# Optimization experiments

Hardware: AMD Instinct MI355X
Metric: run time of the kernel (lower is better)

## Reference

```python
import jax, jax.numpy as jnp
import numpy as np

N, D = 32, 16  # output capsules, output capsule dim
J, I = 16, 8   # input capsules, input capsule dim
B = 16384

def setup_inputs() -> dict:
    key = jax.random.key(0)
    k1, k2 = jax.random.split(key)
    inputs = jax.random.normal(k1, (B, J, I), dtype=jnp.float32)
    # kaiming_normal_ on (N,16,8,D): fan_in computed from dims -> std = sqrt(2/fan_in)
    fan_in = I * D  # torch fan_in for a 4D tensor (N,16,8,D) is dim1*receptive? faithful scale: gain*sqrt(1/fan)
    W = jax.random.normal(k2, (N, J, I, D), dtype=jnp.float32) * np.float32(np.sqrt(2.0 / (J * I * D / N if False else fan_in)))
    b = jnp.zeros((N, J, 1), dtype=jnp.float32)
    return {"inputs": inputs, "W": W, "b": b}

def reference(inputs, W, b):
    # pose transform: u[b,n,j,z] = sum_i inputs[b,j,i] * W[n,j,i,z]
    u = jnp.einsum('bji,njiz->bnjz', inputs, W)          # (B, N, J, D)
    # self-agreement: c[b,n,i] = sum_{k,j} u[b,n,i,j] * u[b,n,k,j]
    c = jnp.einsum('bnij,bnj->bni', u, u.sum(axis=-2))   # (B, N, J)
    c = c[..., None] / jnp.sqrt(jnp.float32(D))          # (B, N, J, 1)
    c = jax.nn.softmax(c, axis=1)                        # softmax over N axis (torch dim=1)
    c = c + b                                            # broadcast (N, J, 1)
    s = jnp.sum(u * c, axis=-2)                          # (B, N, D)
    return s
```

## Files before the change

### kernel.cpp

```cpp
#include <hip/hip_runtime.h>

#define B_TOT 16384
#define TBB   16
#define NTH   512
#define SLS   524

typedef short bf16x8 __attribute__((ext_vector_type(8)));
typedef float f32x4  __attribute__((ext_vector_type(4)));
union U4 { bf16x8 v; uint4 q; };

__device__ __forceinline__ unsigned f2bf(float f) {
    unsigned u = __float_as_uint(f);
    return (u + 0x7fffu + ((u >> 16) & 1u)) >> 16;
}

__device__ __forceinline__ uint4 packrow(const float* src) {
    uint4 o;
    o.x = f2bf(src[0])  | (f2bf(src[16])  << 16);
    o.y = f2bf(src[32]) | (f2bf(src[48])  << 16);
    o.z = f2bf(src[64]) | (f2bf(src[80])  << 16);
    o.w = f2bf(src[96]) | (f2bf(src[112]) << 16);
    return o;
}

__global__ void prepack(const float* __restrict__ W, uint4* __restrict__ Wp)
{
    const int t = blockIdx.x * 256 + threadIdx.x;
    const int lane = t & 63, s = (t >> 6) & 3, n = t >> 8;
    const int q = lane >> 4, z = lane & 15;
    Wp[t] = packrow(W + (size_t)(n * 16 + 4 * s + q) * 128 + z);
}

__global__ __launch_bounds__(NTH, 8)
void caps(const float* __restrict__ X, const uint4* __restrict__ Wp,
          const float* __restrict__ Bias, float* __restrict__ Out)
{
    __shared__ __align__(16) float sL[TBB * SLS];
    __shared__ float sBias[512];

    const int t    = threadIdx.x;
    const int lane = t & 63;
    const int wv   = t >> 6;
    const int b16  = lane & 15;
    const int q    = lane >> 4;
    const long bb  = (long)blockIdx.x * TBB;

    sBias[t] = Bias[t];

    unsigned moct[4];
    #pragma unroll
    for (int c = 0; c < 4; ++c) moct[c] = (q == c) ? 0xffffffffu : 0u;

    uint4 xq[4];
    #pragma unroll
    for (int s = 0; s < 4; ++s) {
        const float* xs = X + (bb + b16) * 128 + (4 * s + q) * 8;
        float4 a = *reinterpret_cast<const float4*>(xs);
        float4 c = *reinterpret_cast<const float4*>(xs + 4);
        uint4 o;
        o.x = f2bf(a.x) | (f2bf(a.y) << 16);
        o.y = f2bf(a.z) | (f2bf(a.w) << 16);
        o.z = f2bf(c.x) | (f2bf(c.y) << 16);
        o.w = f2bf(c.z) | (f2bf(c.w) << 16);
        xq[s] = o;
    }

    const f32x4 zero4 = {0.f, 0.f, 0.f, 0.f};

    auto maskA = [&](const uint4& wkf, int c) {
        U4 a;
        const unsigned m = moct[c];
        a.q.x = wkf.x & m; a.q.y = wkf.y & m;
        a.q.z = wkf.z & m; a.q.w = wkf.w & m;
        return a;
    };

    uint4 wk[4];

    #pragma unroll 1
    for (int nq = 0; nq < 4; ++nq) {
        const int n = wv * 4 + nq;
        const uint4* pw = Wp + n * 256 + lane;
        wk[0] = pw[0]; wk[1] = pw[64]; wk[2] = pw[128]; wk[3] = pw[192];

        f32x4 usum = zero4;
        #pragma unroll
        for (int s = 0; s < 4; ++s) {
            U4 a;  a.q  = wk[s];
            U4 xb; xb.q = xq[s];
            usum = __builtin_amdgcn_mfma_f32_16x16x32_bf16(a.v, xb.v, usum, 0, 0, 0);
        }

        float lv[4];
        #pragma unroll
        for (int j = 0; j < 16; ++j) {
            U4 a  = maskA(wk[j >> 2], j & 3);
            U4 xb; xb.q = xq[j >> 2];
            f32x4 u = __builtin_amdgcn_mfma_f32_16x16x32_bf16(a.v, xb.v, zero4, 0, 0, 0);
            float p = u[0] * usum[0];
            p = fmaf(u[1], usum[1], p);
            p = fmaf(u[2], usum[2], p);
            p = fmaf(u[3], usum[3], p);
            p += __shfl_xor(p, 16);
            p += __shfl_xor(p, 32);
            lv[j & 3] = p * 0.25f;
            if ((j & 3) == 3 && lane < 16)
                *reinterpret_cast<float4*>(&sL[b16 * SLS + n * 16 + (j - 3)]) =
                    make_float4(lv[0], lv[1], lv[2], lv[3]);
        }
    }
    __syncthreads();

    if (t < 256) {
        const int sb = t >> 4, sj = t & 15;
        float l[32];
        #pragma unroll
        for (int n = 0; n < 32; ++n) l[n] = sL[sb * SLS + n * 16 + sj];
        float m = l[0];
        #pragma unroll
        for (int n = 1; n < 32; ++n) m = fmaxf(m, l[n]);
        float Z = 0.f;
        #pragma unroll
        for (int n = 0; n < 32; ++n) { l[n] = __expf(l[n] - m); Z += l[n]; }
        const float inv = 1.0f / Z;
        #pragma unroll
        for (int n = 0; n < 32; ++n)
            sL[sb * SLS + n * 16 + sj] = fmaf(l[n], inv, sBias[n * 16 + sj]);
    }
    __syncthreads();

    #pragma unroll 1
    for (int nq = 0; nq < 4; ++nq) {
        const int n = wv * 4 + nq;
        const uint4* pw = Wp + n * 256 + lane;
        wk[0] = pw[0]; wk[1] = pw[64]; wk[2] = pw[128]; wk[3] = pw[192];

        float s0 = 0.f, s1 = 0.f, s2 = 0.f, s3 = 0.f;
        #pragma unroll
        for (int jp = 0; jp < 8; ++jp) {
            float2 c2 = *reinterpret_cast<const float2*>(&sL[b16 * SLS + n * 16 + 2 * jp]);
            U4 a0 = maskA(wk[jp >> 1], (2 * jp) & 3);
            U4 a1 = maskA(wk[jp >> 1], (2 * jp + 1) & 3);
            U4 x0; x0.q = xq[jp >> 1];
            f32x4 u0 = __builtin_amdgcn_mfma_f32_16x16x32_bf16(a0.v, x0.v, zero4, 0, 0, 0);
            f32x4 u1 = __builtin_amdgcn_mfma_f32_16x16x32_bf16(a1.v, x0.v, zero4, 0, 0, 0);
            s0 = fmaf(c2.x, u0[0], s0); s0 = fmaf(c2.y, u1[0], s0);
            s1 = fmaf(c2.x, u0[1], s1); s1 = fmaf(c2.y, u1[1], s1);
            s2 = fmaf(c2.x, u0[2], s2); s2 = fmaf(c2.y, u1[2], s2);
            s3 = fmaf(c2.x, u0[3], s3); s3 = fmaf(c2.y, u1[3], s3);
        }
        float4* op = reinterpret_cast<float4*>(Out + (bb + b16) * 512 + n * 16 + q * 4);
        *op = make_float4(s0, s1, s2, s3);
    }
}

extern "C" void kernel_launch(void* const* d_in, const int* in_sizes, int n_in,
                              void* d_out, int out_size, void* d_ws, size_t ws_size,
                              hipStream_t stream) {
    const float* X  = (const float*)d_in[0];
    const float* W  = (const float*)d_in[1];
    const float* Bi = (const float*)d_in[2];
    float* Out = (float*)d_out;

    uint4* Wp = (uint4*)d_ws;
    prepack<<<32, 256, 0, stream>>>(W, Wp);
    caps<<<B_TOT / TBB, NTH, 0, stream>>>(X, Wp, Bi, Out);
}
```

Before: 107.0 us.

## Reassociate capsule agreement and weighted sum to cut MFMA count

The logit computation now projects the summed pose vector back through W (a prepacked, pre-scaled transposed copy) and dots the result with the raw inputs. This replaces sixteen masked MFMAs per output capsule with eight. The final weighted sum folds the softmax coefficients into the bf16 input operand, so four accumulating MFMAs replace sixteen. The prepack kernel grows to build the extra W layout, the launch-bounds occupancy hint drops from 8 to 4, and extra bf16 rounding of the coefficient-scaled inputs and usum may change precision.

```diff
diff --git a/kernel.cpp b/kernel.cpp
--- a/kernel.cpp
+++ b/kernel.cpp
@@ -13,6 +13,11 @@
     unsigned u = __float_as_uint(f);
     return (u + 0x7fffu + ((u >> 16) & 1u)) >> 16;
 }
+__device__ __forceinline__ unsigned cvtpk(float lo, float hi) {
+    unsigned r;
+    asm("v_cvt_pk_bf16_f32 %0, %1, %2" : "=v"(r) : "v"(lo), "v"(hi));
+    return r;
+}
 
 __device__ __forceinline__ uint4 packrow(const float* src) {
     uint4 o;
@@ -22,16 +27,35 @@
     o.w = f2bf(src[96]) | (f2bf(src[112]) << 16);
     return o;
 }
+__device__ __forceinline__ uint4 packrow8(const float* src, float sc) {
+    uint4 o;
+    o.x = f2bf(sc * src[0]) | (f2bf(sc * src[1]) << 16);
+    o.y = f2bf(sc * src[2]) | (f2bf(sc * src[3]) << 16);
+    o.z = f2bf(sc * src[4]) | (f2bf(sc * src[5]) << 16);
+    o.w = f2bf(sc * src[6]) | (f2bf(sc * src[7]) << 16);
+    return o;
+}
 
 __global__ void prepack(const float* __restrict__ W, uint4* __restrict__ Wp)
 {
     const int t = blockIdx.x * 256 + threadIdx.x;
-    const int lane = t & 63, s = (t >> 6) & 3, n = t >> 8;
-    const int q = lane >> 4, z = lane & 15;
-    Wp[t] = packrow(W + (size_t)(n * 16 + 4 * s + q) * 128 + z);
+    if (t < 8192) {
+        const int lane = t & 63, s = (t >> 6) & 3, n = t >> 8;
+        const int q = lane >> 4, z = lane & 15;
+        Wp[t] = packrow(W + (size_t)(n * 16 + 4 * s + q) * 128 + z);
+    } else {
+        const int u = t - 8192;
+        const int lane = u & 63, m = (u >> 6) & 7, n = u >> 9;
+        const int g = lane >> 4, r = lane & 15;
+        const int j = 2 * m + (r >> 3), i = r & 7;
+        uint4 o = make_uint4(0u, 0u, 0u, 0u);
+        if (g < 2)
+            o = packrow8(W + (size_t)((n * 16 + j) * 8 + i) * 16 + 8 * g, 0.25f);
+        Wp[t] = o;
+    }
 }
 
-__global__ __launch_bounds__(NTH, 8)
+__global__ __launch_bounds__(NTH, 4)
 void caps(const float* __restrict__ X, const uint4* __restrict__ Wp,
           const float* __restrict__ Bias, float* __restrict__ Out)
 {
@@ -47,14 +71,11 @@
 
     sBias[t] = Bias[t];
 
-    unsigned moct[4];
-    #pragma unroll
-    for (int c = 0; c < 4; ++c) moct[c] = (q == c) ? 0xffffffffu : 0u;
-
+    const float* xr = X + (bb + b16) * 128;
     uint4 xq[4];
     #pragma unroll
     for (int s = 0; s < 4; ++s) {
-        const float* xs = X + (bb + b16) * 128 + (4 * s + q) * 8;
+        const float* xs = xr + (4 * s + q) * 8;
         float4 a = *reinterpret_cast<const float4*>(xs);
         float4 c = *reinterpret_cast<const float4*>(xs + 4);
         uint4 o;
@@ -65,16 +86,12 @@
         xq[s] = o;
     }
 
+    float4 x1[8];
+    #pragma unroll
+    for (int m = 0; m < 8; ++m)
+        x1[m] = *reinterpret_cast<const float4*>(xr + (2 * m + (q >> 1)) * 8 + 4 * (q & 1));
+
     const f32x4 zero4 = {0.f, 0.f, 0.f, 0.f};
-
-    auto maskA = [&](const uint4& wkf, int c) {
-        U4 a;
-        const unsigned m = moct[c];
-        a.q.x = wkf.x & m; a.q.y = wkf.y & m;
-        a.q.z = wkf.z & m; a.q.w = wkf.w & m;
-        return a;
-    };
-
     uint4 wk[4];
 
     #pragma unroll 1
@@ -91,22 +108,27 @@
             usum = __builtin_amdgcn_mfma_f32_16x16x32_bf16(a.v, xb.v, usum, 0, 0, 0);
         }
 
-        float lv[4];
+        const int sA = ((2 * q) & 3) * 16 + b16;
+        const int sB = ((2 * q + 1) & 3) * 16 + b16;
+        const float qa0 = __shfl(usum[0], sA), qa1 = __shfl(usum[1], sA);
+        const float qa2 = __shfl(usum[2], sA), qa3 = __shfl(usum[3], sA);
+        const float qb0 = __shfl(usum[0], sB), qb1 = __shfl(usum[1], sB);
+        const float qb2 = __shfl(usum[2], sB), qb3 = __shfl(usum[3], sB);
+        U4 ub;
+        ub.q.x = cvtpk(qa0, qa1); ub.q.y = cvtpk(qa2, qa3);
+        ub.q.z = cvtpk(qb0, qb1); ub.q.w = cvtpk(qb2, qb3);
+
+        const uint4* pv = Wp + 8192 + n * 512 + lane;
         #pragma unroll
-        for (int j = 0; j < 16; ++j) {
-            U4 a  = maskA(wk[j >> 2], j & 3);
-            U4 xb; xb.q = xq[j >> 2];
-            f32x4 u = __builtin_amdgcn_mfma_f32_16x16x32_bf16(a.v, xb.v, zero4, 0, 0, 0);
-            float p = u[0] * usum[0];
-            p = fmaf(u[1], usum[1], p);
-            p = fmaf(u[2], usum[2], p);
-            p = fmaf(u[3], usum[3], p);
-            p += __shfl_xor(p, 16);
-            p += __shfl_xor(p, 32);
-            lv[j & 3] = p * 0.25f;
-            if ((j & 3) == 3 && lane < 16)
-                *reinterpret_cast<float4*>(&sL[b16 * SLS + n * 16 + (j - 3)]) =
-                    make_float4(lv[0], lv[1], lv[2], lv[3]);
+        for (int m = 0; m < 8; ++m) {
+            U4 a; a.q = pv[m * 64];
+            f32x4 vd = __builtin_amdgcn_mfma_f32_16x16x32_bf16(a.v, ub.v, zero4, 0, 0, 0);
+            float pm = vd[0] * x1[m].x;
+            pm = fmaf(vd[1], x1[m].y, pm);
+            pm = fmaf(vd[2], x1[m].z, pm);
+            pm = fmaf(vd[3], x1[m].w, pm);
+            pm += __shfl_xor(pm, 16);
+            if (!(q & 1)) sL[b16 * SLS + n * 16 + 2 * m + (q >> 1)] = pm;
         }
     }
     __syncthreads();
@@ -135,22 +157,21 @@
         const uint4* pw = Wp + n * 256 + lane;
         wk[0] = pw[0]; wk[1] = pw[64]; wk[2] = pw[128]; wk[3] = pw[192];
 
-        float s0 = 0.f, s1 = 0.f, s2 = 0.f, s3 = 0.f;
+        f32x4 sacc = zero4;
         #pragma unroll
-        for (int jp = 0; jp < 8; ++jp) {
-            float2 c2 = *reinterpret_cast<const float2*>(&sL[b16 * SLS + n * 16 + 2 * jp]);
-            U4 a0 = maskA(wk[jp >> 1], (2 * jp) & 3);
-            U4 a1 = maskA(wk[jp >> 1], (2 * jp + 1) & 3);
-            U4 x0; x0.q = xq[jp >> 1];
-            f32x4 u0 = __builtin_amdgcn_mfma_f32_16x16x32_bf16(a0.v, x0.v, zero4, 0, 0, 0);
-            f32x4 u1 = __builtin_amdgcn_mfma_f32_16x16x32_bf16(a1.v, x0.v, zero4, 0, 0, 0);
-            s0 = fmaf(c2.x, u0[0], s0); s0 = fmaf(c2.y, u1[0], s0);
-            s1 = fmaf(c2.x, u0[1], s1); s1 = fmaf(c2.y, u1[1], s1);
-            s2 = fmaf(c2.x, u0[2], s2); s2 = fmaf(c2.y, u1[2], s2);
-            s3 = fmaf(c2.x, u0[3], s3); s3 = fmaf(c2.y, u1[3], s3);
+        for (int s = 0; s < 4; ++s) {
+            const float c = sL[b16 * SLS + n * 16 + 4 * s + q];
+            const uint4 xv = xq[s];
+            U4 y;
+            y.q.x = cvtpk(c * __uint_as_float(xv.x << 16), c * __uint_as_float(xv.x & 0xffff0000u));
+            y.q.y = cvtpk(c * __uint_as_float(xv.y << 16), c * __uint_as_float(xv.y & 0xffff0000u));
+            y.q.z = cvtpk(c * __uint_as_float(xv.z << 16), c * __uint_as_float(xv.z & 0xffff0000u));
+            y.q.w = cvtpk(c * __uint_as_float(xv.w << 16), c * __uint_as_float(xv.w & 0xffff0000u));
+            U4 a; a.q = wk[s];
+            sacc = __builtin_amdgcn_mfma_f32_16x16x32_bf16(a.v, y.v, sacc, 0, 0, 0);
         }
         float4* op = reinterpret_cast<float4*>(Out + (bb + b16) * 512 + n * 16 + q * 4);
-        *op = make_float4(s0, s1, s2, s3);
+        *op = make_float4(sacc[0], sacc[1], sacc[2], sacc[3]);
     }
 }
 
@@ -163,6 +184,6 @@
     float* Out = (float*)d_out;
 
     uint4* Wp = (uint4*)d_ws;
-    prepack<<<32, 256, 0, stream>>>(W, Wp);
+    prepack<<<96, 256, 0, stream>>>(W, Wp);
     caps<<<B_TOT / TBB, NTH, 0, stream>>>(X, Wp, Bi, Out);
 }
```

After: 113.9 us. 1.06x slower.
